# Kernel tuning notes

Hardware: AMD Instinct MI355X
Metric: run time of the kernel (lower is better)

The kernel has to match this reference:

```python
import jax, jax.numpy as jnp
import numpy as np

N, DIN, H, E, S = 20000, 128, 2048, 2048, 2000
TPM = 0.1        # HP.TIME_PENALTY_MIXING
ENT = 0.01       # HP.ENTROPY_COEF
NEG = -1e30      # finite mask value (avoids -inf NaNs in grads)


def setup_inputs() -> dict:
    key = jax.random.key(0)
    ks = jax.random.split(key, 7)
    feature_vecs = jax.random.normal(ks[0], (N, DIN), dtype=jnp.float32)
    W1 = jax.random.normal(ks[1], (DIN, H), dtype=jnp.float32) * (1.0 / np.sqrt(DIN))
    b1 = jnp.zeros((H,), dtype=jnp.float32)
    W2 = jax.random.normal(ks[2], (H, E), dtype=jnp.float32) * (1.0 / np.sqrt(H))
    b2 = jnp.zeros((E,), dtype=jnp.float32)
    key_vec = jax.random.normal(ks[3], (E,), dtype=jnp.float32) * (1.0 / np.sqrt(E))
    rng = np.random.default_rng(0)
    mask_np = rng.random((S, N)) < 0.4           # passive-set membership per SEL event
    mask_np[:, :2] = True                        # guarantee |passive| >= 2
    good_np = rng.random(N) < 0.05               # proof_flas membership
    r = rng.random((S, N)) * mask_np
    sel_idx_np = r.argmax(axis=1)                # selected clause is inside passive set
    times_np = rng.random(S).astype(np.float32)
    return {
        "feature_vecs": feature_vecs, "W1": W1, "b1": b1, "W2": W2, "b2": b2,
        "key_vec": key_vec,
        "times": jnp.asarray(times_np),
        "mask": jnp.asarray(mask_np),
        "good": jnp.asarray(good_np),
        "sel_idx": jnp.asarray(sel_idx_np, dtype=jnp.int32),
    }


def reference(feature_vecs, W1, b1, W2, b2, key_vec, times, mask, good, sel_idx):
    # clause_embedder: 2-layer MLP; clause_key: dot with key vector -> logits [N]
    h = jax.nn.relu(feature_vecs @ W1 + b1)
    embeddings = h @ W2 + b2                     # [N, E]
    logits = embeddings @ key_vec                # [N]

    # masked log-softmax per SEL event over the passive set
    ml = jnp.where(mask, logits[None, :], NEG)   # [S, N]
    lsm = jax.nn.log_softmax(ml, axis=1)         # [S, N]

    # good-action reward loss (LEARN_FROM_ALL_GOOD)
    gm = mask & good[None, :]                    # good clauses currently passive
    ng = gm.sum(axis=1)                          # [S]
    good_terms = -jnp.where(gm, lsm, 0.0).sum(axis=1)
    has_good = ng > 0
    good_loss = jnp.sum(jnp.where(has_good, good_terms / jnp.maximum(ng, 1), 0.0))
    num_good_steps = has_good.sum()

    # time penalty loss on the selected clause's log-prob
    sel_lsm = jnp.take_along_axis(lsm, sel_idx[:, None], axis=1)[:, 0]
    time_loss = TPM * jnp.sum(times * sel_lsm)
    time_volume = jnp.sum(times)

    # normalized entropy loss
    p = jnp.exp(lsm)
    psz = mask.sum(axis=1).astype(lsm.dtype)
    minus_ent = jnp.where(mask, p * lsm, 0.0).sum(axis=1) / jnp.log(psz)
    entropy_loss = ENT * jnp.sum(minus_ent)
    num_steps = jnp.asarray(S, dtype=jnp.int32)

    return (good_loss, num_good_steps, time_loss, time_volume, entropy_loss, num_steps)
```

## Files before the change

### kernel.cpp

```cpp
#include <hip/hip_runtime.h>

#define NCL 20000
#define DIN 128
#define HID 2048
#define SEVN 2000
#define TPM 0.1f
#define ENTC 0.01f

#define MPAD 20224
#define T64 316

#define NWORD 625
#define CWORDS 5
#define NCHUNK 125
#define EGRP 8
#define SPAD 2048

#define WS_B2K   0
#define WS_W2K   256
#define WS_LOGIT 8448
#define WS_CDATA 89600
#define WS_ASTG  409600
#define WS_BSTG  5586944
#define WS_PACK  6111232
#define WS_PART  11111232

#define NB_PACK 4883
#define NB_SA   1264
#define NB_SB   128
#define NB_WK   513

typedef __attribute__((ext_vector_type(8))) short short8;
typedef __attribute__((ext_vector_type(4))) float f32x4;

static __device__ __forceinline__ unsigned short f2bf(float f) {
    unsigned u = __float_as_uint(f);
    u += 0x7FFFu + ((u >> 16) & 1u);
    return (unsigned short)(u >> 16);
}
static __device__ __forceinline__ unsigned pck(unsigned short a, unsigned short b) {
    return (unsigned)a | ((unsigned)b << 16);
}

__global__ __launch_bounds__(256) void k_stream(const unsigned* __restrict__ mask,
                                                unsigned* __restrict__ packed,
                                                const float* __restrict__ fv,
                                                unsigned short* __restrict__ ast,
                                                const float* __restrict__ W1,
                                                unsigned short* __restrict__ bst,
                                                const float* __restrict__ W2,
                                                const float* __restrict__ b2,
                                                const float* __restrict__ key,
                                                float* __restrict__ w2k,
                                                float* __restrict__ b2k) {
    int b = blockIdx.x;
    int t = threadIdx.x;

    if (b < NB_PACK) {
        int id = b * 256 + t;
        if (id >= SEVN * NWORD) return;
        int s = id / NWORD;
        int w = id - s * NWORD;
        const uint4* p = (const uint4*)(mask + (size_t)s * NCL + w * 32);
        unsigned word = 0;
        #pragma unroll
        for (int q = 0; q < 8; ++q) {
            uint4 m = p[q];
            word |= (m.x ? 1u : 0u) << (q * 4 + 0);
            word |= (m.y ? 1u : 0u) << (q * 4 + 1);
            word |= (m.z ? 1u : 0u) << (q * 4 + 2);
            word |= (m.w ? 1u : 0u) << (q * 4 + 3);
        }
        packed[(size_t)s * NWORD + w] = word;
        return;
    }
    b -= NB_PACK;

    if (b < NB_SA) {
        int g = b * 256 + t;
        int l = g & 63, c = (g >> 6) & 3, s = (g >> 8) & 3, r = g >> 10;
        int row = r * 64 + s * 16 + (l & 15);
        int k0  = c * 32 + (l >> 4) * 8;
        uint4 o;
        if (row < NCL) {
            const float* p = fv + (size_t)row * DIN + k0;
            float4 f0 = *(const float4*)p;
            float4 f1 = *(const float4*)(p + 4);
            o.x = pck(f2bf(f0.x), f2bf(f0.y));
            o.y = pck(f2bf(f0.z), f2bf(f0.w));
            o.z = pck(f2bf(f1.x), f2bf(f1.y));
            o.w = pck(f2bf(f1.z), f2bf(f1.w));
        } else {
            o.x = o.y = o.z = o.w = 0u;
        }
        ((uint4*)ast)[g] = o;
        return;
    }
    b -= NB_SA;

    if (b < NB_SB) {
        int g = b * 256 + t;
        int l = g & 63, c = (g >> 6) & 3, ct = g >> 8;
        int col = ct * 16 + (l & 15);
        int kb  = c * 32 + (l >> 4) * 8;
        unsigned short v[8];
        #pragma unroll
        for (int j = 0; j < 8; ++j) v[j] = f2bf(W1[(size_t)(kb + j) * HID + col]);
        uint4 o;
        o.x = pck(v[0], v[1]); o.y = pck(v[2], v[3]);
        o.z = pck(v[4], v[5]); o.w = pck(v[6], v[7]);
        ((uint4*)bst)[g] = o;
        return;
    }
    b -= NB_SB;

    {
        int wid  = b * 4 + (t >> 6);
        int lane = t & 63;
        const float4* key4 = (const float4*)key;
        float acc = 0.f;
        if (wid <= HID) {
            const float4* row4 = (const float4*)((wid < HID) ? (W2 + (size_t)wid * 2048) : b2);
            #pragma unroll
            for (int it = 0; it < 8; ++it) {
                int idx = it * 64 + lane;
                float4 a = row4[idx], k4 = key4[idx];
                acc += a.x * k4.x + a.y * k4.y + a.z * k4.z + a.w * k4.w;
            }
        }
        #pragma unroll
        for (int m = 1; m < 64; m <<= 1) acc += __shfl_xor(acc, m);
        if (lane == 0 && wid < HID) w2k[wid] = acc;
        if (lane == 0 && wid == HID) *b2k = acc;
    }
}

__global__ __launch_bounds__(512) void k_gemm(const unsigned short* __restrict__ ast,
                                              const unsigned short* __restrict__ bst,
                                              const float* __restrict__ b1,
                                              const float* __restrict__ w2k,
                                              const float* __restrict__ b2k,
                                              const int* __restrict__ good,
                                              float* __restrict__ logits,
                                              float4* __restrict__ cd) {
    int blk = blockIdx.x;
    int tid = threadIdx.x;
    int w = tid >> 6, l = tid & 63;
    int colg = l & 15, kg = l >> 4;

    const short8* A8 = (const short8*)ast;
    const short8* B8 = (const short8*)bst;

    short8 afrag[4][4];
    #pragma unroll
    for (int s = 0; s < 4; ++s) {
        #pragma unroll
        for (int c = 0; c < 4; ++c)
            afrag[s][c] = A8[((((blk * 4 + s) * 4) + c) << 6) + l];
    }

    float acc[4][4];
    #pragma unroll
    for (int s = 0; s < 4; ++s)
        #pragma unroll
        for (int r = 0; r < 4; ++r) acc[s][r] = 0.f;

    int ct0 = w * 16;
    for (int t = 0; t < 16; ++t) {
        int ct = ct0 + t;
        short8 bfr[4];
        #pragma unroll
        for (int c = 0; c < 4; ++c) bfr[c] = B8[((ct * 4 + c) << 6) + l];
        int col = ct * 16 + colg;
        float b1v = b1[col];
        float wkv = w2k[col];
        #pragma unroll
        for (int s = 0; s < 4; ++s) {
            f32x4 d = {0.f, 0.f, 0.f, 0.f};
            #pragma unroll
            for (int c = 0; c < 4; ++c)
                d = __builtin_amdgcn_mfma_f32_16x16x32_bf16(afrag[s][c], bfr[c], d, 0, 0, 0);
            #pragma unroll
            for (int r = 0; r < 4; ++r) {
                float h = d[r] + b1v;
                h = h > 0.f ? h : 0.f;
                acc[s][r] += h * wkv;
            }
        }
    }

    __shared__ float red[8][64];
    #pragma unroll
    for (int s = 0; s < 4; ++s) {
        #pragma unroll
        for (int r = 0; r < 4; ++r) {
            float a = acc[s][r];
            a += __shfl_xor(a, 1);
            a += __shfl_xor(a, 2);
            a += __shfl_xor(a, 4);
            a += __shfl_xor(a, 8);
            if (colg == 0) red[w][s * 16 + kg * 4 + r] = a;
        }
    }
    __syncthreads();
    if (tid < 64) {
        float sum = *b2k;
        #pragma unroll
        for (int ww = 0; ww < 8; ++ww) sum += red[ww][tid];
        int row = blk * 64 + tid;
        logits[row] = sum;
        if (row < NCL) {
            float e = expf(sum);
            bool g = good[row] != 0;
            cd[row] = make_float4(e, e * sum, g ? sum : 0.f, g ? 1.f : 0.f);
        }
    }
}

__global__ __launch_bounds__(256) void k_events(const unsigned* __restrict__ packed,
                                                const float4* __restrict__ cd,
                                                float* __restrict__ part) {
    int chunk = blockIdx.x / EGRP;
    int eg    = blockIdx.x % EGRP;
    int s     = eg * 256 + threadIdx.x;
    float Z = 0.f, X = 0.f, cnt = 0.f, ng = 0.f, sg = 0.f;
    if (s < SEVN) {
        int w0 = chunk * CWORDS;
        unsigned wv[CWORDS];
        #pragma unroll
        for (int w = 0; w < CWORDS; ++w)
            wv[w] = packed[(size_t)s * NWORD + w0 + w];
        #pragma unroll
        for (int w = 0; w < CWORDS; ++w) {
            int cbase = (w0 + w) * 32;
            #pragma unroll
            for (int b = 0; b < 32; ++b) {
                float4 c = cd[cbase + b];
                bool m = (wv[w] >> b) & 1u;
                Z   += m ? c.x : 0.f;
                X   += m ? c.y : 0.f;
                sg  += m ? c.z : 0.f;
                ng  += m ? c.w : 0.f;
                cnt += m ? 1.f : 0.f;
            }
        }
    }
    float* pp = part + (size_t)chunk * 5 * SPAD;
    pp[0 * SPAD + s] = Z;
    pp[1 * SPAD + s] = X;
    pp[2 * SPAD + s] = cnt;
    pp[3 * SPAD + s] = ng;
    pp[4 * SPAD + s] = sg;
}

__global__ __launch_bounds__(256) void k_final(const float* __restrict__ part,
                                               const float* __restrict__ logits,
                                               const float* __restrict__ times,
                                               const int* __restrict__ sel,
                                               float* __restrict__ out) {
    int s = blockIdx.x * 256 + threadIdx.x;
    bool live = s < SEVN;
    float Z = 0.f, X = 0.f, cnt = 0.f, ng = 0.f, sg = 0.f;
    if (live) {
        for (int c = 0; c < NCHUNK; ++c) {
            const float* pp = part + (size_t)c * 5 * SPAD;
            Z   += pp[0 * SPAD + s];
            X   += pp[1 * SPAD + s];
            cnt += pp[2 * SPAD + s];
            ng  += pp[3 * SPAD + s];
            sg  += pp[4 * SPAD + s];
        }
    }
    float gl = 0.f, ngs = 0.f, tl = 0.f, tv = 0.f, en = 0.f;
    if (live) {
        float L = logf(Z);
        if (ng > 0.5f) { gl = L - sg / ng; ngs = 1.f; }
        float tm = times[s];
        tl = TPM * tm * (logits[sel[s]] - L);
        tv = tm;
        en = ENTC * ((X / Z - L) / logf(cnt));
    }
    #pragma unroll
    for (int m = 1; m < 64; m <<= 1) {
        gl  += __shfl_xor(gl, m);
        ngs += __shfl_xor(ngs, m);
        tl  += __shfl_xor(tl, m);
        tv  += __shfl_xor(tv, m);
        en  += __shfl_xor(en, m);
    }
    if ((threadIdx.x & 63) == 0) {
        atomicAdd(out + 0, gl);
        atomicAdd(out + 1, ngs);
        atomicAdd(out + 2, tl);
        atomicAdd(out + 3, tv);
        atomicAdd(out + 4, en);
    }
    if (s == 0) out[5] = (float)SEVN;
}

extern "C" void kernel_launch(void* const* d_in, const int* in_sizes, int n_in,
                              void* d_out, int out_size, void* d_ws, size_t ws_size,
                              hipStream_t stream) {
    const float* fv    = (const float*)d_in[0];
    const float* W1    = (const float*)d_in[1];
    const float* b1    = (const float*)d_in[2];
    const float* W2    = (const float*)d_in[3];
    const float* b2    = (const float*)d_in[4];
    const float* key   = (const float*)d_in[5];
    const float* times = (const float*)d_in[6];
    const unsigned* mask = (const unsigned*)d_in[7];
    const int* good    = (const int*)d_in[8];
    const int* sel     = (const int*)d_in[9];
    float* out = (float*)d_out;
    char* ws = (char*)d_ws;

    float* w2k    = (float*)(ws + WS_W2K);
    float* b2k    = (float*)(ws + WS_B2K);
    float* logits = (float*)(ws + WS_LOGIT);
    float4* cdata = (float4*)(ws + WS_CDATA);
    unsigned short* ast = (unsigned short*)(ws + WS_ASTG);
    unsigned short* bst = (unsigned short*)(ws + WS_BSTG);
    unsigned* packed = (unsigned*)(ws + WS_PACK);
    float* part   = (float*)(ws + WS_PART);

    hipMemsetAsync(d_out, 0, 6 * sizeof(float), stream);
    k_stream<<<NB_PACK + NB_SA + NB_SB + NB_WK, 256, 0, stream>>>(
        mask, packed, fv, ast, W1, bst, W2, b2, key, w2k, b2k);
    k_gemm <<<T64, 512, 0, stream>>>(ast, bst, b1, w2k, b2k, good, logits, cdata);
    k_events<<<NCHUNK * EGRP, 256, 0, stream>>>(packed, cdata, part);
    k_final<<<SPAD / 256, 256, 0, stream>>>(part, logits, times, sel, out);
}
```

Baseline: 327.9 us.

## Pack mask bits with wave ballots and prefetch B fragments in MLP loop

The mask-packing stage now has each wave read 256 consecutive mask words with coalesced loads and build bits with __ballot, in a grid-stride loop over a fixed number of blocks. This replaces the old per-thread strided 128-byte reads. The fused MLP loop now double-buffers the B fragments, bias and w2k values, loading the next tile before computing the current one to hide load latency. The prefetch costs extra registers and may lower occupancy.

Result: no change. 326.5 us (-0.4%).

```diff
diff --git a/kernel.cpp b/kernel.cpp
--- a/kernel.cpp
+++ b/kernel.cpp
@@ -15,6 +15,7 @@
 #define NCHUNK 125
 #define EGRP 8
 #define SPAD 2048
+#define NW_ITERS 156250
 
 #define WS_B2K   0
 #define WS_W2K   256
@@ -25,7 +26,7 @@
 #define WS_PACK  6111232
 #define WS_PART  11111232
 
-#define NB_PACK 4883
+#define NB_PACK 1024
 #define NB_SA   1264
 #define NB_SB   128
 #define NB_WK   513
@@ -57,21 +58,25 @@
     int t = threadIdx.x;
 
     if (b < NB_PACK) {
-        int id = b * 256 + t;
-        if (id >= SEVN * NWORD) return;
-        int s = id / NWORD;
-        int w = id - s * NWORD;
-        const uint4* p = (const uint4*)(mask + (size_t)s * NCL + w * 32);
-        unsigned word = 0;
-        #pragma unroll
-        for (int q = 0; q < 8; ++q) {
-            uint4 m = p[q];
-            word |= (m.x ? 1u : 0u) << (q * 4 + 0);
-            word |= (m.y ? 1u : 0u) << (q * 4 + 1);
-            word |= (m.z ? 1u : 0u) << (q * 4 + 2);
-            word |= (m.w ? 1u : 0u) << (q * 4 + 3);
-        }
-        packed[(size_t)s * NWORD + w] = word;
+        int lane = t & 63;
+        int wid  = b * 4 + (t >> 6);
+        for (int it = wid; it < NW_ITERS; it += NB_PACK * 4) {
+            size_t ibase = (size_t)it * 256;
+            unsigned m0 = mask[ibase +   0 + lane];
+            unsigned m1 = mask[ibase +  64 + lane];
+            unsigned m2 = mask[ibase + 128 + lane];
+            unsigned m3 = mask[ibase + 192 + lane];
+            unsigned long long b0 = __ballot(m0 != 0);
+            unsigned long long b1 = __ballot(m1 != 0);
+            unsigned long long b2_ = __ballot(m2 != 0);
+            unsigned long long b3 = __ballot(m3 != 0);
+            if (lane < 8) {
+                int q = lane >> 1;
+                unsigned long long bq = (q == 0) ? b0 : (q == 1) ? b1 : (q == 2) ? b2_ : b3;
+                unsigned v = (lane & 1) ? (unsigned)(bq >> 32) : (unsigned)bq;
+                packed[(size_t)it * 8 + lane] = v;
+            }
+        }
         return;
     }
     b -= NB_PACK;
@@ -166,26 +171,39 @@
         for (int r = 0; r < 4; ++r) acc[s][r] = 0.f;
 
     int ct0 = w * 16;
+    short8 bcur[4];
+    #pragma unroll
+    for (int c = 0; c < 4; ++c) bcur[c] = B8[((ct0 * 4 + c) << 6) + l];
+    float b1c = b1[ct0 * 16 + colg];
+    float wkc = w2k[ct0 * 16 + colg];
+
     for (int t = 0; t < 16; ++t) {
-        int ct = ct0 + t;
-        short8 bfr[4];
-        #pragma unroll
-        for (int c = 0; c < 4; ++c) bfr[c] = B8[((ct * 4 + c) << 6) + l];
-        int col = ct * 16 + colg;
-        float b1v = b1[col];
-        float wkv = w2k[col];
+        short8 bnxt[4];
+        float b1n = 0.f, wkn = 0.f;
+        if (t < 15) {
+            int ctn = ct0 + t + 1;
+            #pragma unroll
+            for (int c = 0; c < 4; ++c) bnxt[c] = B8[((ctn * 4 + c) << 6) + l];
+            b1n = b1[ctn * 16 + colg];
+            wkn = w2k[ctn * 16 + colg];
+        }
         #pragma unroll
         for (int s = 0; s < 4; ++s) {
             f32x4 d = {0.f, 0.f, 0.f, 0.f};
             #pragma unroll
             for (int c = 0; c < 4; ++c)
-                d = __builtin_amdgcn_mfma_f32_16x16x32_bf16(afrag[s][c], bfr[c], d, 0, 0, 0);
+                d = __builtin_amdgcn_mfma_f32_16x16x32_bf16(afrag[s][c], bcur[c], d, 0, 0, 0);
             #pragma unroll
             for (int r = 0; r < 4; ++r) {
-                float h = d[r] + b1v;
+                float h = d[r] + b1c;
                 h = h > 0.f ? h : 0.f;
-                acc[s][r] += h * wkv;
+                acc[s][r] += h * wkc;
             }
+        }
+        if (t < 15) {
+            #pragma unroll
+            for (int c = 0; c < 4; ++c) bcur[c] = bnxt[c];
+            b1c = b1n; wkc = wkn;
         }
     }
 
```

## Pack mask with wave ballots, fuse A-staging into GEMM, regroup event chunks

Applied to the files above, without the earlier changes.

Mask packing now uses coalesced wave-wide loads and __ballot to build bit words per 256-clause group. This replaces per-thread 128-byte strided reads and uses a grid-stride job loop. The separate bf16 staging pass for feature vectors is removed, and k_gemm converts fp32 rows to bf16 fragments directly. k_gemm now uses 32-row tiles with 256 threads (625 blocks) instead of 64-row tiles. The event reduction is reorganised into 79 groups to match the new packed bit layout, with a special tail case for the last partial group.

Measured after the change: 358.3 us. +9.3%, slower.

```diff
diff --git a/kernel.cpp b/kernel.cpp
--- a/kernel.cpp
+++ b/kernel.cpp
@@ -7,26 +7,20 @@
 #define TPM 0.1f
 #define ENTC 0.01f
 
-#define MPAD 20224
-#define T64 316
-
-#define NWORD 625
-#define CWORDS 5
-#define NCHUNK 125
-#define EGRP 8
+#define RG 79
+#define NJOBS (SEVN * RG)
+#define LASTJOB (NJOBS - 1)
 #define SPAD 2048
 
 #define WS_B2K   0
 #define WS_W2K   256
 #define WS_LOGIT 8448
 #define WS_CDATA 89600
-#define WS_ASTG  409600
-#define WS_BSTG  5586944
-#define WS_PACK  6111232
-#define WS_PART  11111232
-
-#define NB_PACK 4883
-#define NB_SA   1264
+#define WS_BSTG  409600
+#define WS_PACK  933888
+#define WS_PART  5989888
+
+#define NB_PACK 2048
 #define NB_SB   128
 #define NB_WK   513
 
@@ -44,8 +38,6 @@
 
 __global__ __launch_bounds__(256) void k_stream(const unsigned* __restrict__ mask,
                                                 unsigned* __restrict__ packed,
-                                                const float* __restrict__ fv,
-                                                unsigned short* __restrict__ ast,
                                                 const float* __restrict__ W1,
                                                 unsigned short* __restrict__ bst,
                                                 const float* __restrict__ W2,
@@ -57,46 +49,29 @@
     int t = threadIdx.x;
 
     if (b < NB_PACK) {
-        int id = b * 256 + t;
-        if (id >= SEVN * NWORD) return;
-        int s = id / NWORD;
-        int w = id - s * NWORD;
-        const uint4* p = (const uint4*)(mask + (size_t)s * NCL + w * 32);
-        unsigned word = 0;
-        #pragma unroll
-        for (int q = 0; q < 8; ++q) {
-            uint4 m = p[q];
-            word |= (m.x ? 1u : 0u) << (q * 4 + 0);
-            word |= (m.y ? 1u : 0u) << (q * 4 + 1);
-            word |= (m.z ? 1u : 0u) << (q * 4 + 2);
-            word |= (m.w ? 1u : 0u) << (q * 4 + 3);
-        }
-        packed[(size_t)s * NWORD + w] = word;
+        int lane = t & 63;
+        int wv   = b * 4 + (t >> 6);
+        for (int job = wv; job < NJOBS; job += NB_PACK * 4) {
+            int s  = job / RG;
+            int gr = job - s * RG;
+            const unsigned* gp = mask + (size_t)s * NCL + gr * 256;
+            int off = 4 * lane;
+            if (job == LASTJOB && lane >= 8) off = 0;
+            uint4 m = *(const uint4*)(gp + off);
+            unsigned long long B0 = __ballot(m.x != 0);
+            unsigned long long B1 = __ballot(m.y != 0);
+            unsigned long long B2 = __ballot(m.z != 0);
+            unsigned long long B3 = __ballot(m.w != 0);
+            if (lane < 8) {
+                int k = lane >> 1;
+                unsigned long long Bk = (k == 0) ? B0 : (k == 1) ? B1 : (k == 2) ? B2 : B3;
+                unsigned v = (lane & 1) ? (unsigned)(Bk >> 32) : (unsigned)Bk;
+                packed[(size_t)job * 8 + lane] = v;
+            }
+        }
         return;
     }
     b -= NB_PACK;
-
-    if (b < NB_SA) {
-        int g = b * 256 + t;
-        int l = g & 63, c = (g >> 6) & 3, s = (g >> 8) & 3, r = g >> 10;
-        int row = r * 64 + s * 16 + (l & 15);
-        int k0  = c * 32 + (l >> 4) * 8;
-        uint4 o;
-        if (row < NCL) {
-            const float* p = fv + (size_t)row * DIN + k0;
-            float4 f0 = *(const float4*)p;
-            float4 f1 = *(const float4*)(p + 4);
-            o.x = pck(f2bf(f0.x), f2bf(f0.y));
-            o.y = pck(f2bf(f0.z), f2bf(f0.w));
-            o.z = pck(f2bf(f1.x), f2bf(f1.y));
-            o.w = pck(f2bf(f1.z), f2bf(f1.w));
-        } else {
-            o.x = o.y = o.z = o.w = 0u;
-        }
-        ((uint4*)ast)[g] = o;
-        return;
-    }
-    b -= NB_SA;
 
     if (b < NB_SB) {
         int g = b * 256 + t;
@@ -135,7 +110,7 @@
     }
 }
 
-__global__ __launch_bounds__(512) void k_gemm(const unsigned short* __restrict__ ast,
+__global__ __launch_bounds__(256) void k_gemm(const float* __restrict__ fv,
                                               const unsigned short* __restrict__ bst,
                                               const float* __restrict__ b1,
                                               const float* __restrict__ w2k,
@@ -147,26 +122,35 @@
     int tid = threadIdx.x;
     int w = tid >> 6, l = tid & 63;
     int colg = l & 15, kg = l >> 4;
-
-    const short8* A8 = (const short8*)ast;
+    int r0 = blk * 32;
+
     const short8* B8 = (const short8*)bst;
 
-    short8 afrag[4][4];
+    short8 afrag[2][4];
     #pragma unroll
-    for (int s = 0; s < 4; ++s) {
-        #pragma unroll
-        for (int c = 0; c < 4; ++c)
-            afrag[s][c] = A8[((((blk * 4 + s) * 4) + c) << 6) + l];
-    }
-
-    float acc[4][4];
+    for (int s = 0; s < 2; ++s) {
+        const float* rp = fv + (size_t)(r0 + s * 16 + (l & 15)) * DIN + kg * 8;
+        #pragma unroll
+        for (int c = 0; c < 4; ++c) {
+            float4 f0 = *(const float4*)(rp + c * 32);
+            float4 f1 = *(const float4*)(rp + c * 32 + 4);
+            union { short8 sv; uint4 u; } tmp;
+            tmp.u.x = pck(f2bf(f0.x), f2bf(f0.y));
+            tmp.u.y = pck(f2bf(f0.z), f2bf(f0.w));
+            tmp.u.z = pck(f2bf(f1.x), f2bf(f1.y));
+            tmp.u.w = pck(f2bf(f1.z), f2bf(f1.w));
+            afrag[s][c] = tmp.sv;
+        }
+    }
+
+    float acc[2][4];
     #pragma unroll
-    for (int s = 0; s < 4; ++s)
+    for (int s = 0; s < 2; ++s)
         #pragma unroll
         for (int r = 0; r < 4; ++r) acc[s][r] = 0.f;
 
-    int ct0 = w * 16;
-    for (int t = 0; t < 16; ++t) {
+    int ct0 = w * 32;
+    for (int t = 0; t < 32; ++t) {
         int ct = ct0 + t;
         short8 bfr[4];
         #pragma unroll
@@ -175,7 +159,7 @@
         float b1v = b1[col];
         float wkv = w2k[col];
         #pragma unroll
-        for (int s = 0; s < 4; ++s) {
+        for (int s = 0; s < 2; ++s) {
             f32x4 d = {0.f, 0.f, 0.f, 0.f};
             #pragma unroll
             for (int c = 0; c < 4; ++c)
@@ -189,9 +173,9 @@
         }
     }
 
-    __shared__ float red[8][64];
+    __shared__ float red[4][32];
     #pragma unroll
-    for (int s = 0; s < 4; ++s) {
+    for (int s = 0; s < 2; ++s) {
         #pragma unroll
         for (int r = 0; r < 4; ++r) {
             float a = acc[s][r];
@@ -203,49 +187,69 @@
         }
     }
     __syncthreads();
-    if (tid < 64) {
+    if (tid < 32) {
         float sum = *b2k;
         #pragma unroll
-        for (int ww = 0; ww < 8; ++ww) sum += red[ww][tid];
-        int row = blk * 64 + tid;
+        for (int ww = 0; ww < 4; ++ww) sum += red[ww][tid];
+        int row = r0 + tid;
         logits[row] = sum;
-        if (row < NCL) {
-            float e = expf(sum);
-            bool g = good[row] != 0;
-            cd[row] = make_float4(e, e * sum, g ? sum : 0.f, g ? 1.f : 0.f);
-        }
+        float e = expf(sum);
+        bool g = good[row] != 0;
+        cd[row] = make_float4(e, e * sum, g ? sum : 0.f, g ? 1.f : 0.f);
     }
 }
 
 __global__ __launch_bounds__(256) void k_events(const unsigned* __restrict__ packed,
                                                 const float4* __restrict__ cd,
                                                 float* __restrict__ part) {
-    int chunk = blockIdx.x / EGRP;
-    int eg    = blockIdx.x % EGRP;
-    int s     = eg * 256 + threadIdx.x;
+    int gr = blockIdx.x >> 3;
+    int eg = blockIdx.x & 7;
+    int s  = eg * 256 + threadIdx.x;
     float Z = 0.f, X = 0.f, cnt = 0.f, ng = 0.f, sg = 0.f;
     if (s < SEVN) {
-        int w0 = chunk * CWORDS;
-        unsigned wv[CWORDS];
-        #pragma unroll
-        for (int w = 0; w < CWORDS; ++w)
-            wv[w] = packed[(size_t)s * NWORD + w0 + w];
-        #pragma unroll
-        for (int w = 0; w < CWORDS; ++w) {
-            int cbase = (w0 + w) * 32;
-            #pragma unroll
-            for (int b = 0; b < 32; ++b) {
-                float4 c = cd[cbase + b];
-                bool m = (wv[w] >> b) & 1u;
-                Z   += m ? c.x : 0.f;
-                X   += m ? c.y : 0.f;
-                sg  += m ? c.z : 0.f;
-                ng  += m ? c.w : 0.f;
-                cnt += m ? 1.f : 0.f;
-            }
-        }
-    }
-    float* pp = part + (size_t)chunk * 5 * SPAD;
+        const unsigned* wp = packed + ((size_t)s * RG + gr) * 8;
+        unsigned wv[8];
+        #pragma unroll
+        for (int j = 0; j < 8; ++j) wv[j] = wp[j];
+        int cbase = gr * 256;
+        if (gr < RG - 1) {
+            #pragma unroll
+            for (int k = 0; k < 4; ++k) {
+                #pragma unroll
+                for (int half = 0; half < 2; ++half) {
+                    unsigned word = wv[2 * k + half];
+                    int cb = cbase + 128 * half + k;
+                    #pragma unroll
+                    for (int b = 0; b < 32; ++b) {
+                        float4 c = cd[cb + 4 * b];
+                        float m = (float)((word >> b) & 1u);
+                        Z   += m * c.x;
+                        X   += m * c.y;
+                        sg  += m * c.z;
+                        ng  += m * c.w;
+                        cnt += m;
+                    }
+                }
+            }
+        } else {
+            #pragma unroll
+            for (int k = 0; k < 4; ++k) {
+                unsigned word = wv[2 * k];
+                int cb = cbase + k;
+                #pragma unroll
+                for (int b = 0; b < 8; ++b) {
+                    float4 c = cd[cb + 4 * b];
+                    float m = (float)((word >> b) & 1u);
+                    Z   += m * c.x;
+                    X   += m * c.y;
+                    sg  += m * c.z;
+                    ng  += m * c.w;
+                    cnt += m;
+                }
+            }
+        }
+    }
+    float* pp = part + (size_t)gr * 5 * SPAD;
     pp[0 * SPAD + s] = Z;
     pp[1 * SPAD + s] = X;
     pp[2 * SPAD + s] = cnt;
@@ -262,7 +266,7 @@
     bool live = s < SEVN;
     float Z = 0.f, X = 0.f, cnt = 0.f, ng = 0.f, sg = 0.f;
     if (live) {
-        for (int c = 0; c < NCHUNK; ++c) {
+        for (int c = 0; c < RG; ++c) {
             const float* pp = part + (size_t)c * 5 * SPAD;
             Z   += pp[0 * SPAD + s];
             X   += pp[1 * SPAD + s];
@@ -318,15 +322,14 @@
     float* b2k    = (float*)(ws + WS_B2K);
     float* logits = (float*)(ws + WS_LOGIT);
     float4* cdata = (float4*)(ws + WS_CDATA);
-    unsigned short* ast = (unsigned short*)(ws + WS_ASTG);
     unsigned short* bst = (unsigned short*)(ws + WS_BSTG);
     unsigned* packed = (unsigned*)(ws + WS_PACK);
     float* part   = (float*)(ws + WS_PART);
 
     hipMemsetAsync(d_out, 0, 6 * sizeof(float), stream);
-    k_stream<<<NB_PACK + NB_SA + NB_SB + NB_WK, 256, 0, stream>>>(
-        mask, packed, fv, ast, W1, bst, W2, b2, key, w2k, b2k);
-    k_gemm <<<T64, 512, 0, stream>>>(ast, bst, b1, w2k, b2k, good, logits, cdata);
-    k_events<<<NCHUNK * EGRP, 256, 0, stream>>>(packed, cdata, part);
+    k_stream<<<NB_PACK + NB_SB + NB_WK, 256, 0, stream>>>(
+        mask, packed, W1, bst, W2, b2, key, w2k, b2k);
+    k_gemm <<<NCL / 32, 256, 0, stream>>>(fv, bst, b1, w2k, b2k, good, logits, cdata);
+    k_events<<<RG * 8, 256, 0, stream>>>(packed, cdata, part);
     k_final<<<SPAD / 256, 256, 0, stream>>>(part, logits, times, sel, out);
 }
```
